# Kernel tuning notes

Hardware: AMD Instinct MI355X
Metric: run time of the kernel (lower is better)

Reference implementation:

```python
import jax, jax.numpy as jnp
import numpy as np

ALPHA = 1.702  # ORT swiglu activation constant


def setup_inputs() -> dict:
    key = jax.random.key(0)
    ks = jax.random.split(key, 6)
    B, S, H, I, E = 4, 1024, 2048, 2048, 8
    return {
        "hidden_states": jax.random.normal(ks[0], (B, S, H), dtype=jnp.float32),
        "gate_w": jax.random.normal(ks[1], (E, H), dtype=jnp.float32) * 0.02,
        "fc1_w": jax.random.normal(ks[2], (E, 2 * I, H), dtype=jnp.float32) * 0.02,
        "fc1_b": jax.random.normal(ks[3], (E, 2 * I), dtype=jnp.float32) * 0.02,
        "fc2_w": jax.random.normal(ks[4], (E, H, I), dtype=jnp.float32) * 0.02,
        "fc2_b": jax.random.normal(ks[5], (E, H), dtype=jnp.float32) * 0.02,
        "top_k": 2,
    }


def reference(hidden_states, gate_w, fc1_w, fc1_b, fc2_w, fc2_b, top_k):
    B, S, H = hidden_states.shape
    E = gate_w.shape[0]
    x = hidden_states.reshape(-1, H)                      # [T, H]
    T = x.shape[0]

    # Router: softmax -> top-k -> renormalize selected weights
    logits = jnp.einsum("th,eh->te", x, gate_w)           # [T, E]
    probs = jax.nn.softmax(logits, axis=-1)
    top_vals, top_idx = jax.lax.top_k(probs, top_k)       # [T, k]
    top_vals = top_vals / jnp.sum(top_vals, axis=-1, keepdims=True)
    # Dense combine weights [T, E] (zero for non-selected experts)
    combine = jnp.zeros((T, E), dtype=x.dtype).at[
        jnp.arange(T)[:, None], top_idx
    ].add(top_vals)

    # Expert FC1 (packed gate/linear, interleaved) -> swiglu -> FC2
    h = jnp.einsum("th,efh->etf", x, fc1_w) + fc1_b[:, None, :]   # [E, T, 2I]
    g = h[..., 0::2]                                              # gate part [E, T, I]
    l = h[..., 1::2]                                              # linear part [E, T, I]
    a = g * jax.nn.sigmoid(ALPHA * g) * (l + 1.0)                 # [E, T, I]
    y = jnp.einsum("eti,ehi->eth", a, fc2_w) + fc2_b[:, None, :]  # [E, T, H]

    out = jnp.einsum("te,eth->th", combine, y)            # weighted combine
    return out.reshape(B, S, H)
```

## Files before the change

### kernel.cpp

```cpp
#include <hip/hip_runtime.h>
#include <math.h>


#define T_TOK 4096
#define H_DIM 2048
#define I_DIM 2048
#define F_DIM 4096
#define E_NUM 8
#define ALPHA_C 1.702f
#define ALPHA_LOG2E 2.4554674f

#define TILE_M 64
#define KT 32
#define ACT_CAP_F (2 * T_TOK + E_NUM * TILE_M)
#define BTM 128
#define ACT_CAP_B (2 * T_TOK + E_NUM * BTM)

#define GATE_BLOCKS (T_TOK / 4)
#define CVT_BLOCKS 1024
#define CHUNK_F4 2048
#define NCHUNK 12288
#define W1_CHUNKS 8192
#define W1_F4 16777216
#define CVT_ITERS (NCHUNK / CVT_BLOCKS)

typedef unsigned short ushort_t;
typedef __attribute__((ext_vector_type(8))) unsigned short ushort8v;
typedef __attribute__((ext_vector_type(8))) __bf16 bf16x8;
typedef __attribute__((ext_vector_type(4))) float f32x4;

__device__ __forceinline__ ushort_t f2bf(float f) {
    unsigned int u = __float_as_uint(f);
    unsigned int r = (u + 0x7FFFu + ((u >> 16) & 1u)) >> 16;
    return (ushort_t)r;
}
__device__ __forceinline__ float bf2f(ushort_t b) {
    return __uint_as_float(((unsigned int)b) << 16);
}

__device__ __forceinline__ void gl_lds16(const ushort_t* g, ushort_t* l) {
    __builtin_amdgcn_global_load_lds(
        (const __attribute__((address_space(1))) void*)g,
        (__attribute__((address_space(3))) void*)l, 16, 0, 0);
}

__global__ __launch_bounds__(256) void prep_kernel(
    const float* __restrict__ x, const float* __restrict__ gw,
    const float* __restrict__ w1, const float* __restrict__ w2,
    ushort_t* __restrict__ wb, ushort_t* __restrict__ xb,
    int* __restrict__ tok, int4* __restrict__ tidx, float2* __restrict__ twgt,
    int* __restrict__ cnt) {
    if (blockIdx.x < GATE_BLOCKS) {
        int t = blockIdx.x * 4 + (threadIdx.x >> 6);
        int lane = threadIdx.x & 63;
        const float* xr = x + (size_t)t * H_DIM;
        ushort_t* xbr = xb + (size_t)t * H_DIM;
        float acc[E_NUM];
#pragma unroll
        for (int e = 0; e < E_NUM; e++) acc[e] = 0.f;
#pragma unroll
        for (int i = 0; i < H_DIM / 256; i++) {
            int j = (i * 64 + lane) * 4;
            float4 xv = *(const float4*)(xr + j);
            *(ushort4*)(xbr + j) =
                make_ushort4(f2bf(xv.x), f2bf(xv.y), f2bf(xv.z), f2bf(xv.w));
#pragma unroll
            for (int e = 0; e < E_NUM; e++) {
                float4 g = *(const float4*)(gw + e * H_DIM + j);
                acc[e] += xv.x * g.x + xv.y * g.y + xv.z * g.z + xv.w * g.w;
            }
        }
#pragma unroll
        for (int e = 0; e < E_NUM; e++) {
#pragma unroll
            for (int s = 32; s > 0; s >>= 1) acc[e] += __shfl_xor(acc[e], s, 64);
        }
        if (lane == 0) {
            int i0 = 0; float b0 = acc[0];
            for (int e = 1; e < E_NUM; e++) if (acc[e] > b0) { b0 = acc[e]; i0 = e; }
            int i1 = -1; float b1 = -3.0e38f;
            for (int e = 0; e < E_NUM; e++) {
                if (e == i0) continue;
                if (acc[e] > b1) { b1 = acc[e]; i1 = e; }
            }
            float e10 = expf(b1 - b0);
            float w0 = 1.f / (1.f + e10);
            float w1v = 1.f - w0;
            int p0 = atomicAdd(&cnt[i0], 1);
            tok[i0 * T_TOK + p0] = t;
            int p1 = atomicAdd(&cnt[i1], 1);
            tok[i1 * T_TOK + p1] = t;
            tidx[t] = make_int4(i0, p0, i1, p1);
            twgt[t] = make_float2(w0, w1v);
        }
    } else {
        int bid = (int)blockIdx.x - GATE_BLOCKS;
        int tid = (int)threadIdx.x;
        for (int i = 0; i < CVT_ITERS; i++) {
            int c = bid + i * CVT_BLOCKS;
            size_t g0 = (size_t)c * CHUNK_F4 + tid;
            const float* s = (c < W1_CHUNKS)
                                 ? (w1 + g0 * 4)
                                 : (w2 + (g0 - (size_t)W1_F4) * 4);
            ushort_t* d = wb + g0 * 4;
            f32x4 v[8];
#pragma unroll
            for (int j = 0; j < 8; j++)
                v[j] = *(const f32x4*)(s + (size_t)j * 1024);
#pragma unroll
            for (int j = 0; j < 8; j++) {
                *(ushort4*)(d + (size_t)j * 1024) = make_ushort4(
                    f2bf(v[j][0]), f2bf(v[j][1]), f2bf(v[j][2]), f2bf(v[j][3]));
            }
        }
    }
}

__device__ __forceinline__ void calc_off(const int* __restrict__ cnt, int e,
                                         int& off_e, int& cpad_e) {
    int o = 0, cp = 0;
#pragma unroll
    for (int q = 0; q < E_NUM; q++) {
        int c = (cnt[q] + BTM - 1) & ~(BTM - 1);
        if (q < e) o += c;
        if (q == e) cp = c;
    }
    off_e = o; cpad_e = cp;
}

__global__ __launch_bounds__(256, 3) void fc1_mfma(
    const ushort_t* __restrict__ xb, const ushort_t* __restrict__ w1b,
    const float* __restrict__ b1, const int* __restrict__ tok,
    const int* __restrict__ cnt, ushort_t* __restrict__ act) {
    int e = blockIdx.y >> 5;
    int tile = blockIdx.y & 31;
    int off_e, cpad_e;
    calc_off(cnt, e, off_e, cpad_e);
    if (tile * BTM >= cpad_e) return;
    int i0 = blockIdx.x * 64;

    __shared__ ushort_t As[2][128 * 32];
    __shared__ ushort_t Bg[2][64 * 32];
    __shared__ ushort_t Bl[2][64 * 32];

    int tid = threadIdx.x;
    int lane = tid & 63;
    int ww = tid >> 6;
    int wm = ww & 1, wn = ww >> 1;
    int l15 = lane & 15, quad = lane >> 4;
    int r4 = lane >> 2;
    int koff = (lane & 3) * 8;

    const int* tlist = tok + e * T_TOK + tile * BTM;
    int ar0 = ww * 32 + r4;
    const ushort_t* a0 = xb + (size_t)tlist[ar0] * H_DIM + koff;
    const ushort_t* a1 = xb + (size_t)tlist[ar0 + 16] * H_DIM + koff;
    int il = ww * 16 + r4;
    const ushort_t* bsrc = w1b + ((size_t)e * F_DIM + 2 * (i0 + il)) * H_DIM + koff;

    ushort_t* ad0a = &As[0][(ww * 32) * 32];
    ushort_t* ad0b = &As[0][(ww * 32 + 16) * 32];
    ushort_t* ad1a = &As[1][(ww * 32) * 32];
    ushort_t* ad1b = &As[1][(ww * 32 + 16) * 32];
    ushort_t* bg0 = &Bg[0][(ww * 16) * 32];
    ushort_t* bg1 = &Bg[1][(ww * 16) * 32];
    ushort_t* bl0 = &Bl[0][(ww * 16) * 32];
    ushort_t* bl1 = &Bl[1][(ww * 16) * 32];

    f32x4 zf = {0.f, 0.f, 0.f, 0.f};
    f32x4 accg[4][2], accl[4][2];
#pragma unroll
    for (int mc = 0; mc < 4; mc++)
#pragma unroll
        for (int nc = 0; nc < 2; nc++) { accg[mc][nc] = zf; accl[mc][nc] = zf; }

    for (int k0 = 0; k0 < H_DIM; k0 += 64) {
        __syncthreads();
        gl_lds16(a0, ad0a);
        gl_lds16(a1, ad0b);
        gl_lds16(a0 + 32, ad1a);
        gl_lds16(a1 + 32, ad1b);
        gl_lds16(bsrc, bg0);
        gl_lds16(bsrc + 32, bg1);
        gl_lds16(bsrc + H_DIM, bl0);
        gl_lds16(bsrc + H_DIM + 32, bl1);
        a0 += 64; a1 += 64; bsrc += 64;
        __syncthreads();

#pragma unroll
        for (int kk = 0; kk < 2; kk++) {
            bf16x8 af[4], bgf[2], blf[2];
#pragma unroll
            for (int mc = 0; mc < 4; mc++)
                af[mc] = *(const bf16x8*)&As[kk][(wm * 64 + mc * 16 + l15) * 32 + quad * 8];
#pragma unroll
            for (int nc = 0; nc < 2; nc++) {
                bgf[nc] = *(const bf16x8*)&Bg[kk][(wn * 32 + nc * 16 + l15) * 32 + quad * 8];
                blf[nc] = *(const bf16x8*)&Bl[kk][(wn * 32 + nc * 16 + l15) * 32 + quad * 8];
            }
#pragma unroll
            for (int mc = 0; mc < 4; mc++)
#pragma unroll
                for (int nc = 0; nc < 2; nc++) {
                    accg[mc][nc] = __builtin_amdgcn_mfma_f32_16x16x32_bf16(
                        af[mc], bgf[nc], accg[mc][nc], 0, 0, 0);
                    accl[mc][nc] = __builtin_amdgcn_mfma_f32_16x16x32_bf16(
                        af[mc], blf[nc], accl[mc][nc], 0, 0, 0);
                }
        }
    }

    int rowbase = off_e + tile * BTM + wm * 64;
    int colbase = i0 + wn * 32;
    float bgc[2], blc[2];
#pragma unroll
    for (int nc = 0; nc < 2; nc++) {
        int i = colbase + nc * 16 + l15;
        bgc[nc] = b1[(size_t)e * F_DIM + 2 * i];
        blc[nc] = b1[(size_t)e * F_DIM + 2 * i + 1];
    }
#pragma unroll
    for (int mc = 0; mc < 4; mc++)
#pragma unroll
        for (int nc = 0; nc < 2; nc++) {
            int i = colbase + nc * 16 + l15;
#pragma unroll
            for (int r = 0; r < 4; r++) {
                int m = rowbase + mc * 16 + quad * 4 + r;
                float g = accg[mc][nc][r] + bgc[nc];
                float l = accl[mc][nc][r] + blc[nc];
                float s = __builtin_amdgcn_rcpf(
                    1.f + __builtin_amdgcn_exp2f(-ALPHA_LOG2E * g));
                act[(size_t)m * I_DIM + i] = f2bf(g * s * (l + 1.f));
            }
        }
}

__global__ __launch_bounds__(256, 3) void fc2_mfma(
    const ushort_t* __restrict__ act, const ushort_t* __restrict__ w2b,
    const float* __restrict__ b2, const int* __restrict__ cnt,
    ushort_t* __restrict__ ybuf) {
    int e = blockIdx.y >> 5;
    int tile = blockIdx.y & 31;
    int off_e, cpad_e;
    calc_off(cnt, e, off_e, cpad_e);
    if (tile * BTM >= cpad_e) return;
    int h0 = blockIdx.x * 128;
    int rowbase = off_e + tile * BTM;

    __shared__ ushort_t As[2][128 * 32];
    __shared__ ushort_t Bs[2][128 * 32];

    int tid = threadIdx.x;
    int lane = tid & 63;
    int ww = tid >> 6;
    int wm = ww & 1, wn = ww >> 1;
    int l15 = lane & 15, quad = lane >> 4;
    int r4 = lane >> 2;
    int koff = (lane & 3) * 8;

    int ar = ww * 32 + r4;
    const ushort_t* a0 = act + (size_t)(rowbase + ar) * I_DIM + koff;
    const ushort_t* a1 = a0 + (size_t)16 * I_DIM;
    const ushort_t* b0 = w2b + ((size_t)e * H_DIM + h0 + ar) * I_DIM + koff;
    const ushort_t* b1p = b0 + (size_t)16 * I_DIM;

    ushort_t* ad0a = &As[0][(ww * 32) * 32];
    ushort_t* ad0b = &As[0][(ww * 32 + 16) * 32];
    ushort_t* ad1a = &As[1][(ww * 32) * 32];
    ushort_t* ad1b = &As[1][(ww * 32 + 16) * 32];
    ushort_t* bd0a = &Bs[0][(ww * 32) * 32];
    ushort_t* bd0b = &Bs[0][(ww * 32 + 16) * 32];
    ushort_t* bd1a = &Bs[1][(ww * 32) * 32];
    ushort_t* bd1b = &Bs[1][(ww * 32 + 16) * 32];

    f32x4 zf = {0.f, 0.f, 0.f, 0.f};
    f32x4 acc[4][4];
#pragma unroll
    for (int mc = 0; mc < 4; mc++)
#pragma unroll
        for (int nc = 0; nc < 4; nc++) acc[mc][nc] = zf;

    for (int k0 = 0; k0 < I_DIM; k0 += 64) {
        __syncthreads();
        gl_lds16(a0, ad0a);
        gl_lds16(a1, ad0b);
        gl_lds16(a0 + 32, ad1a);
        gl_lds16(a1 + 32, ad1b);
        gl_lds16(b0, bd0a);
        gl_lds16(b1p, bd0b);
        gl_lds16(b0 + 32, bd1a);
        gl_lds16(b1p + 32, bd1b);
        a0 += 64; a1 += 64; b0 += 64; b1p += 64;
        __syncthreads();

#pragma unroll
        for (int kk = 0; kk < 2; kk++) {
            bf16x8 af[4], bf[4];
#pragma unroll
            for (int mc = 0; mc < 4; mc++)
                af[mc] = *(const bf16x8*)&As[kk][(wm * 64 + mc * 16 + l15) * 32 + quad * 8];
#pragma unroll
            for (int nc = 0; nc < 4; nc++)
                bf[nc] = *(const bf16x8*)&Bs[kk][(wn * 64 + nc * 16 + l15) * 32 + quad * 8];
#pragma unroll
            for (int mc = 0; mc < 4; mc++)
#pragma unroll
                for (int nc = 0; nc < 4; nc++)
                    acc[mc][nc] = __builtin_amdgcn_mfma_f32_16x16x32_bf16(
                        af[mc], bf[nc], acc[mc][nc], 0, 0, 0);
        }
    }

    float bc[4];
#pragma unroll
    for (int nc = 0; nc < 4; nc++)
        bc[nc] = b2[(size_t)e * H_DIM + h0 + wn * 64 + nc * 16 + l15];
#pragma unroll
    for (int mc = 0; mc < 4; mc++)
#pragma unroll
        for (int nc = 0; nc < 4; nc++) {
            int h = h0 + wn * 64 + nc * 16 + l15;
#pragma unroll
            for (int r = 0; r < 4; r++) {
                int m = rowbase + wm * 64 + mc * 16 + quad * 4 + r;
                ybuf[(size_t)m * H_DIM + h] = f2bf(acc[mc][nc][r] + bc[nc]);
            }
        }
}

__global__ __launch_bounds__(256) void combine_kernel(
    const ushort_t* __restrict__ ybuf, const int4* __restrict__ tidx,
    const float2* __restrict__ twgt, const int* __restrict__ cnt,
    float* __restrict__ out) {
    int offv[E_NUM];
    {
        int o = 0;
#pragma unroll
        for (int q = 0; q < E_NUM; q++) {
            offv[q] = o;
            o += (cnt[q] + BTM - 1) & ~(BTM - 1);
        }
    }
    int h = threadIdx.x * 8;
#pragma unroll
    for (int tt = 0; tt < 4; tt++) {
        int t = blockIdx.x * 4 + tt;
        int4 idx = tidx[t];
        float2 w = twgt[t];
        size_t r0 = (size_t)offv[idx.x] + idx.y;
        size_t r1 = (size_t)offv[idx.z] + idx.w;
        ushort8v a = *(const ushort8v*)(ybuf + r0 * H_DIM + h);
        ushort8v b = *(const ushort8v*)(ybuf + r1 * H_DIM + h);
        float* op = out + (size_t)t * H_DIM + h;
#pragma unroll
        for (int q = 0; q < 8; q++)
            op[q] = w.x * bf2f(a[q]) + w.y * bf2f(b[q]);
    }
}

__global__ __launch_bounds__(64) void gate_fb(
    const float* __restrict__ x, const float* __restrict__ gw,
    int* __restrict__ tok, float* __restrict__ wgt,
    int4* __restrict__ tidx, float2* __restrict__ twgt, int* __restrict__ cnt) {
    int t = blockIdx.x;
    int lane = threadIdx.x;
    const float* xr = x + (size_t)t * H_DIM;
    float acc[E_NUM];
#pragma unroll
    for (int e = 0; e < E_NUM; e++) acc[e] = 0.f;
    for (int j = lane; j < H_DIM; j += 64) {
        float xv = xr[j];
#pragma unroll
        for (int e = 0; e < E_NUM; e++) acc[e] += xv * gw[e * H_DIM + j];
    }
#pragma unroll
    for (int e = 0; e < E_NUM; e++) {
#pragma unroll
        for (int s = 32; s > 0; s >>= 1) acc[e] += __shfl_xor(acc[e], s, 64);
    }
    if (lane == 0) {
        int i0 = 0; float b0 = acc[0];
        for (int e = 1; e < E_NUM; e++) if (acc[e] > b0) { b0 = acc[e]; i0 = e; }
        int i1 = -1; float b1 = -3.0e38f;
        for (int e = 0; e < E_NUM; e++) {
            if (e == i0) continue;
            if (acc[e] > b1) { b1 = acc[e]; i1 = e; }
        }
        float e10 = expf(b1 - b0);
        float w0 = 1.f / (1.f + e10);
        float w1 = 1.f - w0;
        int p0 = atomicAdd(&cnt[i0], 1);
        tok[i0 * T_TOK + p0] = t; wgt[i0 * T_TOK + p0] = w0;
        int p1 = atomicAdd(&cnt[i1], 1);
        tok[i1 * T_TOK + p1] = t; wgt[i1 * T_TOK + p1] = w1;
        tidx[t] = make_int4(i0, p0, i1, p1);
        twgt[t] = make_float2(w0, w1);
    }
}

__global__ __launch_bounds__(256) void pad_kernel(
    int* __restrict__ tok, float* __restrict__ wgt,
    const int* __restrict__ cnt, int* __restrict__ cnt_pad,
    int* __restrict__ off, int tile) {
    __shared__ int s_cnt[E_NUM], s_pad[E_NUM];
    if (threadIdx.x == 0) {
        int o = 0;
        for (int e = 0; e < E_NUM; e++) {
            int c = cnt[e];
            int cp = (c + tile - 1) / tile * tile;
            s_cnt[e] = c; s_pad[e] = cp;
            cnt_pad[e] = cp;
            off[e] = o;
            o += cp;
        }
    }
    __syncthreads();
    for (int e = 0; e < E_NUM; e++) {
        for (int p = s_cnt[e] + (int)threadIdx.x; p < s_pad[e]; p += 256) {
            tok[e * T_TOK + p] = 0;
            wgt[e * T_TOK + p] = 0.f;
        }
    }
}

__global__ __launch_bounds__(256) void fc1_kernel(
    const float* __restrict__ x, const float* __restrict__ w1,
    const float* __restrict__ b1, const int* __restrict__ tok,
    const int* __restrict__ cnt_pad, const int* __restrict__ off,
    ushort_t* __restrict__ act) {
    int e = blockIdx.y >> 6;
    int tile = blockIdx.y & 63;
    if (tile * TILE_M >= cnt_pad[e]) return;
    int i0 = blockIdx.x * 64;
    int f0 = i0 * 2;

    __shared__ float xs[KT][TILE_M + 4];
    __shared__ float wsh[KT][128 + 4];

    int tid = threadIdx.x;
    int tx = tid & 15, ty = tid >> 4;
    int rloc = tid >> 3;
    int c4 = (tid & 7) * 4;

    const int* tlist = tok + e * T_TOK + tile * TILE_M;
    int tk0 = tlist[rloc];
    int tk1 = tlist[rloc + 32];
    const float* xp0 = x + (size_t)tk0 * H_DIM + c4;
    const float* xp1 = x + (size_t)tk1 * H_DIM + c4;
    const float* wp = w1 + ((size_t)e * F_DIM + f0 + rloc) * H_DIM + c4;

    float ga[4][4] = {{0.f}}, la[4][4] = {{0.f}};

    for (int k0 = 0; k0 < H_DIM; k0 += KT) {
        __syncthreads();
        {
            float4 v0 = *(const float4*)(xp0 + k0);
            float4 v1 = *(const float4*)(xp1 + k0);
            xs[c4 + 0][rloc] = v0.x; xs[c4 + 1][rloc] = v0.y;
            xs[c4 + 2][rloc] = v0.z; xs[c4 + 3][rloc] = v0.w;
            xs[c4 + 0][rloc + 32] = v1.x; xs[c4 + 1][rloc + 32] = v1.y;
            xs[c4 + 2][rloc + 32] = v1.z; xs[c4 + 3][rloc + 32] = v1.w;
        }
        {
#pragma unroll
            for (int r = 0; r < 4; r++) {
                float4 v = *(const float4*)(wp + (size_t)(32 * r) * H_DIM + k0);
                int fr = rloc + 32 * r;
                wsh[c4 + 0][fr] = v.x; wsh[c4 + 1][fr] = v.y;
                wsh[c4 + 2][fr] = v.z; wsh[c4 + 3][fr] = v.w;
            }
        }
        __syncthreads();
#pragma unroll
        for (int k = 0; k < KT; k++) {
            float4 xv = *(const float4*)&xs[k][ty * 4];
            float4 wa = *(const float4*)&wsh[k][tx * 8];
            float4 wb = *(const float4*)&wsh[k][tx * 8 + 4];
            float xm[4] = {xv.x, xv.y, xv.z, xv.w};
            float gg[4] = {wa.x, wa.z, wb.x, wb.z};
            float ll[4] = {wa.y, wa.w, wb.y, wb.w};
#pragma unroll
            for (int m = 0; m < 4; m++)
#pragma unroll
                for (int n = 0; n < 4; n++) {
                    ga[m][n] += xm[m] * gg[n];
                    la[m][n] += xm[m] * ll[n];
                }
        }
    }

    int rowbase = off[e] + tile * TILE_M;
    float bg[4], bl[4];
#pragma unroll
    for (int n = 0; n < 4; n++) {
        int i = i0 + tx * 4 + n;
        bg[n] = b1[(size_t)e * F_DIM + 2 * i];
        bl[n] = b1[(size_t)e * F_DIM + 2 * i + 1];
    }
#pragma unroll
    for (int m = 0; m < 4; m++) {
        int row = rowbase + ty * 4 + m;
        ushort_t us[4];
#pragma unroll
        for (int n = 0; n < 4; n++) {
            float g = ga[m][n] + bg[n];
            float l = la[m][n] + bl[n];
            float s = 1.f / (1.f + expf(-ALPHA_C * g));
            us[n] = f2bf(g * s * (l + 1.f));
        }
        *(ushort4*)&act[(size_t)row * I_DIM + i0 + tx * 4] =
            make_ushort4(us[0], us[1], us[2], us[3]);
    }
}

__global__ __launch_bounds__(256) void fc2_kernel(
    const ushort_t* __restrict__ act, const float* __restrict__ w2,
    const float* __restrict__ b2, const int* __restrict__ tok,
    const float* __restrict__ wgt, const int* __restrict__ cnt_pad,
    const int* __restrict__ off, float* __restrict__ out) {
    int e = blockIdx.y >> 6;
    int tile = blockIdx.y & 63;
    if (tile * TILE_M >= cnt_pad[e]) return;
    int h0 = blockIdx.x * 64;

    __shared__ float as_[KT][TILE_M + 4];
    __shared__ float wsh[KT][64 + 4];

    int tid = threadIdx.x;
    int tx = tid & 15, ty = tid >> 4;
    int rowbase = off[e] + tile * TILE_M;

    int arow = tid >> 2;
    int ac8 = (tid & 3) * 8;
    const ushort_t* ap = act + (size_t)(rowbase + arow) * I_DIM + ac8;
    int rloc = tid >> 3;
    int c4 = (tid & 7) * 4;
    const float* wp = w2 + ((size_t)e * H_DIM + h0 + rloc) * I_DIM + c4;

    float acc[4][4] = {{0.f}};

    for (int k0 = 0; k0 < I_DIM; k0 += KT) {
        __syncthreads();
        {
            ushort8v v = *(const ushort8v*)(ap + k0);
#pragma unroll
            for (int q = 0; q < 8; q++) as_[ac8 + q][arow] = bf2f(v[q]);
        }
        {
#pragma unroll
            for (int r = 0; r < 2; r++) {
                float4 v = *(const float4*)(wp + (size_t)(32 * r) * I_DIM + k0);
                int hr = rloc + 32 * r;
                wsh[c4 + 0][hr] = v.x; wsh[c4 + 1][hr] = v.y;
                wsh[c4 + 2][hr] = v.z; wsh[c4 + 3][hr] = v.w;
            }
        }
        __syncthreads();
#pragma unroll
        for (int k = 0; k < KT; k++) {
            float4 xv = *(const float4*)&as_[k][ty * 4];
            float4 wv = *(const float4*)&wsh[k][tx * 4];
            float xm[4] = {xv.x, xv.y, xv.z, xv.w};
            float wn[4] = {wv.x, wv.y, wv.z, wv.w};
#pragma unroll
            for (int m = 0; m < 4; m++)
#pragma unroll
                for (int n = 0; n < 4; n++) acc[m][n] += xm[m] * wn[n];
        }
    }

    const int* tlist = tok + e * T_TOK + tile * TILE_M;
    const float* wlist = wgt + e * T_TOK + tile * TILE_M;
#pragma unroll
    for (int m = 0; m < 4; m++) {
        int row = ty * 4 + m;
        int t = tlist[row];
        float w = wlist[row];
        if (w == 0.f) continue;
#pragma unroll
        for (int n = 0; n < 4; n++) {
            int h = h0 + tx * 4 + n;
            float y = acc[m][n] + b2[(size_t)e * H_DIM + h];
            atomicAdd(out + (size_t)t * H_DIM + h, w * y);
        }
    }
}

extern "C" void kernel_launch(void* const* d_in, const int* in_sizes, int n_in,
                              void* d_out, int out_size, void* d_ws, size_t ws_size,
                              hipStream_t stream) {
    const float* x  = (const float*)d_in[0];
    const float* gw = (const float*)d_in[1];
    const float* w1 = (const float*)d_in[2];
    const float* b1 = (const float*)d_in[3];
    const float* w2 = (const float*)d_in[4];
    const float* b2 = (const float*)d_in[5];
    float* out = (float*)d_out;
    char* ws = (char*)d_ws;

    size_t w1b_sz = (size_t)E_NUM * F_DIM * H_DIM * 2;
    size_t w2b_sz = (size_t)E_NUM * H_DIM * I_DIM * 2;
    size_t xb_sz  = (size_t)T_TOK * H_DIM * 2;
    size_t act_sz = (size_t)ACT_CAP_B * I_DIM * 2;
    size_t tok_sz = (size_t)E_NUM * T_TOK * 4;
    size_t tidx_sz = (size_t)T_TOK * 16;
    size_t twgt_sz = (size_t)T_TOK * 8;
    size_t need_big = w1b_sz + w2b_sz + xb_sz + act_sz + tok_sz + 64 +
                      tidx_sz + twgt_sz + 256;

    if (ws_size >= need_big) {
        ushort_t* w1b = (ushort_t*)ws;
        ushort_t* w2b = (ushort_t*)(ws + w1b_sz);
        ushort_t* xb  = (ushort_t*)(ws + w1b_sz + w2b_sz);
        ushort_t* act = (ushort_t*)(ws + w1b_sz + w2b_sz + xb_sz);
        char* p = ws + w1b_sz + w2b_sz + xb_sz + act_sz;
        int*    tok  = (int*)p;                 p += tok_sz;
        int*    cnt  = (int*)p;                 p += 64;
        int4*   tidx = (int4*)p;                p += tidx_sz;
        float2* twgt = (float2*)p;
        ushort_t* ybuf = w1b;

        hipMemsetAsync(tok, 0, tok_sz + 64, stream);
        prep_kernel<<<GATE_BLOCKS + CVT_BLOCKS, 256, 0, stream>>>(
            x, gw, w1, w2, w1b, xb, tok, tidx, twgt, cnt);
        fc1_mfma<<<dim3(I_DIM / 64, E_NUM * 32), 256, 0, stream>>>(
            xb, w1b, b1, tok, cnt, act);
        fc2_mfma<<<dim3(H_DIM / 128, E_NUM * 32), 256, 0, stream>>>(
            act, w2b, b2, cnt, ybuf);
        combine_kernel<<<T_TOK / 4, 256, 0, stream>>>(ybuf, tidx, twgt, cnt, out);
        return;
    }

    size_t actB = (size_t)ACT_CAP_F * I_DIM * 2;
    ushort_t* act = (ushort_t*)ws;
    char* p = ws + actB;
    int*    tok  = (int*)p;     p += tok_sz;
    float*  wgt  = (float*)p;   p += tok_sz;
    int4*   tidx = (int4*)p;    p += tidx_sz;
    float2* twgt = (float2*)p;  p += twgt_sz;
    int*    cnt  = (int*)p;
    int*    cnt_pad = cnt + E_NUM;
    int*    off  = cnt_pad + E_NUM;
    size_t need = actB + 2 * tok_sz + tidx_sz + twgt_sz + 256;
    if (ws_size < need) return;

    hipMemsetAsync(cnt, 0, E_NUM * sizeof(int), stream);
    hipMemsetAsync(d_out, 0, (size_t)T_TOK * H_DIM * sizeof(float), stream);
    gate_fb<<<T_TOK, 64, 0, stream>>>(x, gw, tok, wgt, tidx, twgt, cnt);
    pad_kernel<<<1, 256, 0, stream>>>(tok, wgt, cnt, cnt_pad, off, TILE_M);
    fc1_kernel<<<dim3(I_DIM / 64, E_NUM * 64), 256, 0, stream>>>(
        x, w1, b1, tok, cnt_pad, off, act);
    fc2_kernel<<<dim3(H_DIM / 64, E_NUM * 64), 256, 0, stream>>>(
        act, w2, b2, tok, wgt, cnt_pad, off, out);
}
```

Before: 842.2 us.

## Split prep into gate, deterministic ballot-based routing, and weight conversion kernels

The fused prep kernel is split into three launches. The gate kernel computes router logits and top-2 selection without atomics. A new per-expert route kernel builds the token lists in token order using ballot and prefix sums, replacing the atomicAdd-based scatter. Weight conversion becomes its own kernel with twice as many blocks. This removes atomic contention and gives ordered, deterministic token lists that may help FC1 gather locality, at the cost of two extra launches and serialized phases that previously overlapped inside one grid.

```diff
diff --git a/kernel.cpp b/kernel.cpp
--- a/kernel.cpp
+++ b/kernel.cpp
@@ -17,11 +17,11 @@
 #define ACT_CAP_B (2 * T_TOK + E_NUM * BTM)
 
 #define GATE_BLOCKS (T_TOK / 4)
-#define CVT_BLOCKS 1024
 #define CHUNK_F4 2048
 #define NCHUNK 12288
 #define W1_CHUNKS 8192
 #define W1_F4 16777216
+#define CVT_BLOCKS 2048
 #define CVT_ITERS (NCHUNK / CVT_BLOCKS)
 
 typedef unsigned short ushort_t;
@@ -44,74 +44,109 @@
         (__attribute__((address_space(3))) void*)l, 16, 0, 0);
 }
 
-__global__ __launch_bounds__(256) void prep_kernel(
+__global__ __launch_bounds__(256) void gate_kernel(
     const float* __restrict__ x, const float* __restrict__ gw,
+    ushort_t* __restrict__ xb, int4* __restrict__ tidx,
+    float2* __restrict__ twgt) {
+    int t = blockIdx.x * 4 + (threadIdx.x >> 6);
+    int lane = threadIdx.x & 63;
+    const float* xr = x + (size_t)t * H_DIM;
+    ushort_t* xbr = xb + (size_t)t * H_DIM;
+    float acc[E_NUM];
+#pragma unroll
+    for (int e = 0; e < E_NUM; e++) acc[e] = 0.f;
+#pragma unroll
+    for (int i = 0; i < H_DIM / 256; i++) {
+        int j = (i * 64 + lane) * 4;
+        float4 xv = *(const float4*)(xr + j);
+        *(ushort4*)(xbr + j) =
+            make_ushort4(f2bf(xv.x), f2bf(xv.y), f2bf(xv.z), f2bf(xv.w));
+#pragma unroll
+        for (int e = 0; e < E_NUM; e++) {
+            float4 g = *(const float4*)(gw + e * H_DIM + j);
+            acc[e] += xv.x * g.x + xv.y * g.y + xv.z * g.z + xv.w * g.w;
+        }
+    }
+#pragma unroll
+    for (int e = 0; e < E_NUM; e++) {
+#pragma unroll
+        for (int s = 32; s > 0; s >>= 1) acc[e] += __shfl_xor(acc[e], s, 64);
+    }
+    if (lane == 0) {
+        int i0 = 0; float b0 = acc[0];
+        for (int e = 1; e < E_NUM; e++) if (acc[e] > b0) { b0 = acc[e]; i0 = e; }
+        int i1 = -1; float b1 = -3.0e38f;
+        for (int e = 0; e < E_NUM; e++) {
+            if (e == i0) continue;
+            if (acc[e] > b1) { b1 = acc[e]; i1 = e; }
+        }
+        float e10 = expf(b1 - b0);
+        float w0 = 1.f / (1.f + e10);
+        float w1v = 1.f - w0;
+        tidx[t] = make_int4(i0, 0, i1, 0);
+        twgt[t] = make_float2(w0, w1v);
+    }
+}
+
+__global__ __launch_bounds__(256) void route_kernel(
+    const int4* tidx_ro, int* tidx_w, int* __restrict__ tok,
+    int* __restrict__ cnt) {
+    int e = blockIdx.x;
+    int tid = threadIdx.x;
+    int lane = tid & 63;
+    int wv = tid >> 6;
+    __shared__ int wsum[4];
+    __shared__ int sbase;
+    if (tid == 0) sbase = 0;
+    __syncthreads();
+    for (int c = 0; c < T_TOK / 256; c++) {
+        int t = c * 256 + tid;
+        int4 v = tidx_ro[t];
+        bool fA = (v.x == e);
+        bool fB = (v.z == e);
+        bool f = fA || fB;
+        unsigned long long m = __ballot(f);
+        int my = __popcll(m & ((1ull << lane) - 1ull));
+        int wt = __popcll(m);
+        if (lane == 0) wsum[wv] = wt;
+        __syncthreads();
+        int woff = 0;
+#pragma unroll
+        for (int q = 0; q < 4; q++) woff += (q < wv) ? wsum[q] : 0;
+        int tot = wsum[0] + wsum[1] + wsum[2] + wsum[3];
+        int base = sbase;
+        if (f) {
+            int p = base + woff + my;
+            tok[e * T_TOK + p] = t;
+            tidx_w[t * 4 + (fA ? 1 : 3)] = p;
+        }
+        __syncthreads();
+        if (tid == 0) sbase = base + tot;
+        __syncthreads();
+    }
+    if (tid == 0) cnt[e] = sbase;
+}
+
+__global__ __launch_bounds__(256) void cvt_kernel(
     const float* __restrict__ w1, const float* __restrict__ w2,
-    ushort_t* __restrict__ wb, ushort_t* __restrict__ xb,
-    int* __restrict__ tok, int4* __restrict__ tidx, float2* __restrict__ twgt,
-    int* __restrict__ cnt) {
-    if (blockIdx.x < GATE_BLOCKS) {
-        int t = blockIdx.x * 4 + (threadIdx.x >> 6);
-        int lane = threadIdx.x & 63;
-        const float* xr = x + (size_t)t * H_DIM;
-        ushort_t* xbr = xb + (size_t)t * H_DIM;
-        float acc[E_NUM];
-#pragma unroll
-        for (int e = 0; e < E_NUM; e++) acc[e] = 0.f;
-#pragma unroll
-        for (int i = 0; i < H_DIM / 256; i++) {
-            int j = (i * 64 + lane) * 4;
-            float4 xv = *(const float4*)(xr + j);
-            *(ushort4*)(xbr + j) =
-                make_ushort4(f2bf(xv.x), f2bf(xv.y), f2bf(xv.z), f2bf(xv.w));
-#pragma unroll
-            for (int e = 0; e < E_NUM; e++) {
-                float4 g = *(const float4*)(gw + e * H_DIM + j);
-                acc[e] += xv.x * g.x + xv.y * g.y + xv.z * g.z + xv.w * g.w;
-            }
-        }
-#pragma unroll
-        for (int e = 0; e < E_NUM; e++) {
-#pragma unroll
-            for (int s = 32; s > 0; s >>= 1) acc[e] += __shfl_xor(acc[e], s, 64);
-        }
-        if (lane == 0) {
-            int i0 = 0; float b0 = acc[0];
-            for (int e = 1; e < E_NUM; e++) if (acc[e] > b0) { b0 = acc[e]; i0 = e; }
-            int i1 = -1; float b1 = -3.0e38f;
-            for (int e = 0; e < E_NUM; e++) {
-                if (e == i0) continue;
-                if (acc[e] > b1) { b1 = acc[e]; i1 = e; }
-            }
-            float e10 = expf(b1 - b0);
-            float w0 = 1.f / (1.f + e10);
-            float w1v = 1.f - w0;
-            int p0 = atomicAdd(&cnt[i0], 1);
-            tok[i0 * T_TOK + p0] = t;
-            int p1 = atomicAdd(&cnt[i1], 1);
-            tok[i1 * T_TOK + p1] = t;
-            tidx[t] = make_int4(i0, p0, i1, p1);
-            twgt[t] = make_float2(w0, w1v);
-        }
-    } else {
-        int bid = (int)blockIdx.x - GATE_BLOCKS;
-        int tid = (int)threadIdx.x;
-        for (int i = 0; i < CVT_ITERS; i++) {
-            int c = bid + i * CVT_BLOCKS;
-            size_t g0 = (size_t)c * CHUNK_F4 + tid;
-            const float* s = (c < W1_CHUNKS)
-                                 ? (w1 + g0 * 4)
-                                 : (w2 + (g0 - (size_t)W1_F4) * 4);
-            ushort_t* d = wb + g0 * 4;
-            f32x4 v[8];
-#pragma unroll
-            for (int j = 0; j < 8; j++)
-                v[j] = *(const f32x4*)(s + (size_t)j * 1024);
-#pragma unroll
-            for (int j = 0; j < 8; j++) {
-                *(ushort4*)(d + (size_t)j * 1024) = make_ushort4(
-                    f2bf(v[j][0]), f2bf(v[j][1]), f2bf(v[j][2]), f2bf(v[j][3]));
-            }
+    ushort_t* __restrict__ wb) {
+    int bid = (int)blockIdx.x;
+    int tid = (int)threadIdx.x;
+    for (int i = 0; i < CVT_ITERS; i++) {
+        int c = bid + i * CVT_BLOCKS;
+        size_t g0 = (size_t)c * CHUNK_F4 + tid;
+        const float* s = (c < W1_CHUNKS)
+                             ? (w1 + g0 * 4)
+                             : (w2 + (g0 - (size_t)W1_F4) * 4);
+        ushort_t* d = wb + g0 * 4;
+        f32x4 v[8];
+#pragma unroll
+        for (int j = 0; j < 8; j++)
+            v[j] = *(const f32x4*)(s + (size_t)j * 1024);
+#pragma unroll
+        for (int j = 0; j < 8; j++) {
+            *(ushort4*)(d + (size_t)j * 1024) = make_ushort4(
+                f2bf(v[j][0]), f2bf(v[j][1]), f2bf(v[j][2]), f2bf(v[j][3]));
         }
     }
 }
@@ -622,8 +657,10 @@
         ushort_t* ybuf = w1b;
 
         hipMemsetAsync(tok, 0, tok_sz + 64, stream);
-        prep_kernel<<<GATE_BLOCKS + CVT_BLOCKS, 256, 0, stream>>>(
-            x, gw, w1, w2, w1b, xb, tok, tidx, twgt, cnt);
+        gate_kernel<<<GATE_BLOCKS, 256, 0, stream>>>(x, gw, xb, tidx, twgt);
+        route_kernel<<<E_NUM, 256, 0, stream>>>(
+            (const int4*)tidx, (int*)tidx, tok, cnt);
+        cvt_kernel<<<CVT_BLOCKS, 256, 0, stream>>>(w1, w2, w1b);
         fc1_mfma<<<dim3(I_DIM / 64, E_NUM * 32), 256, 0, stream>>>(
             xb, w1b, b1, tok, cnt, act);
         fc2_mfma<<<dim3(H_DIM / 128, E_NUM * 32), 256, 0, stream>>>(
```

After: 791.3 us. -6.0%, faster.
